# Kernel tuning notes

Hardware: AMD Instinct MI355X
Metric: run time of the kernel (lower is better)

## Reference

```python
import jax, jax.numpy as jnp
import numpy as np

B, L, H = 256, 256, 1024
NUM_HEADS = 16
DIM_PER_HEAD = H // NUM_HEADS  # 64
# faithful to source: scale = (dim_per_head // num_heads) ** -0.5 = (64//16)**-0.5 = 0.5
SCALE = (DIM_PER_HEAD // NUM_HEADS) ** (-0.5)
LN_EPS = 1e-5


def setup_inputs() -> dict:
    key = jax.random.key(0)
    ks = jax.random.split(key, 12)
    s = 1.0 / np.sqrt(H)
    return {
        "key": jax.random.normal(ks[0], (B, L, H), dtype=jnp.float32),
        "value": jax.random.normal(ks[1], (B, L, H), dtype=jnp.float32),
        "query": jax.random.normal(ks[2], (B, 1, H), dtype=jnp.float32),
        "attn_mask": jax.random.randint(ks[3], (B, 1, L), 0, 2).astype(bool),
        "Wq": jax.random.uniform(ks[4], (H, H), jnp.float32, -s, s),
        "bq": jnp.zeros((H,), jnp.float32),
        "Wk": jax.random.uniform(ks[5], (H, H), jnp.float32, -s, s),
        "bk": jnp.zeros((H,), jnp.float32),
        "Wv": jax.random.uniform(ks[6], (H, H), jnp.float32, -s, s),
        "bv": jnp.zeros((H,), jnp.float32),
        "Wf": jax.random.uniform(ks[7], (H, H), jnp.float32, -s, s),
        "bf": jnp.zeros((H,), jnp.float32),
        "gamma": jnp.ones((H,), jnp.float32),
        "beta": jnp.zeros((H,), jnp.float32),
    }


def _split_heads(x):
    # [B, L, H] -> [B, heads, L, d]
    b, l, _ = x.shape
    return x.reshape(b, l, NUM_HEADS, DIM_PER_HEAD).transpose(0, 2, 1, 3)


def reference(key, value, query, attn_mask, Wq, bq, Wk, bk, Wv, bv, Wf, bf, gamma, beta):
    residual = query  # [B, 1, H]
    k = _split_heads(key @ Wk.T + bk)      # [B, h, L, d]
    v = _split_heads(value @ Wv.T + bv)    # [B, h, L, d]
    q = _split_heads(query @ Wq.T + bq)    # [B, h, 1, d]

    scores = jnp.einsum('bhqd,bhkd->bhqk', q, k) * SCALE  # [B, h, 1, L]
    mask = attn_mask[:, None, :, :]                       # [B, 1, 1, L]
    scores = jnp.where(mask, -jnp.inf, scores)
    attention = jax.nn.softmax(scores, axis=-1)           # [B, h, 1, L]

    context = jnp.einsum('bhqk,bhkd->bhqd', attention, v)  # [B, h, 1, d]
    context = context.transpose(0, 2, 1, 3).reshape(query.shape[0], -1, H)  # [B, 1, H]

    out = context @ Wf.T + bf
    x = residual + out
    mu = jnp.mean(x, axis=-1, keepdims=True)
    var = jnp.mean(jnp.square(x - mu), axis=-1, keepdims=True)
    out = (x - mu) * jax.lax.rsqrt(var + LN_EPS) * gamma + beta

    # attention returned as [B*heads, 1, L] like torch bmm layout
    attn_flat = attention.reshape(query.shape[0] * NUM_HEADS, 1, -1)
    return out, attn_flat
```

## Files before the change

kernel.cpp:

```cpp
#include <hip/hip_runtime.h>
#include <math.h>

#define BB 256
#define LL 256
#define HH 1024
#define NH 16
#define DD 64
#define SCALE 0.5f
#define LN_EPS 1e-5f
#define NEG_BIG (-3.402823466e38f)

__global__ __launch_bounds__(256) void t_tr(const float* __restrict__ in,
                                            float* __restrict__ out, int inRS,
                                            int outRS, int inPlane,
                                            int outPlane) {
  __shared__ float lds[64][68];
  const float* ip = in + (size_t)blockIdx.z * inPlane;
  float* op = out + (size_t)blockIdx.z * outPlane;
  const int rt = blockIdx.y, ct = blockIdx.x;
  const int lr = threadIdx.x >> 4;
  const int lc = (threadIdx.x & 15) * 4;
#pragma unroll
  for (int p = 0; p < 4; p++) {
    float4 v = *(const float4*)(ip + (size_t)(rt * 64 + p * 16 + lr) * inRS +
                                ct * 64 + lc);
    *(float4*)(&lds[p * 16 + lr][lc]) = v;
  }
  __syncthreads();
#pragma unroll
  for (int p = 0; p < 4; p++) {
    float4 v = make_float4(lds[lc + 0][p * 16 + lr], lds[lc + 1][p * 16 + lr],
                           lds[lc + 2][p * 16 + lr], lds[lc + 3][p * 16 + lr]);
    *(float4*)(op + (size_t)(ct * 64 + p * 16 + lr) * outRS + rt * 64 + lc) = v;
  }
}

__global__ __launch_bounds__(256) void k1_qproj(const float* __restrict__ Wq,
                                                const float* __restrict__ qTT,
                                                const float* __restrict__ bq,
                                                float* __restrict__ qT) {
  __shared__ float smem[10240];
  const int jt = blockIdx.x;
  const int boff = blockIdx.y * 8;
  const int t = threadIdx.x;
  const int g = __builtin_amdgcn_readfirstlane(t >> 6);
  const int ln = t & 63;
  float* kw = smem + g * 2560;
  const float* Wb = Wq + (size_t)(jt * 64) * HH;
  const int srow = ln >> 2, sc = ln & 3;

  float acc[8];
#pragma unroll
  for (int c = 0; c < 8; c++) acc[c] = 0.f;
  float4 pf[4];
#pragma unroll
  for (int p = 0; p < 4; p++)
    pf[p] = *(const float4*)(Wb + (size_t)(p * 16 + srow) * HH + g * 16 + sc * 4);
  int buf = 0;
  for (int T = 0; T < 16; T++) {
    float* kb = kw + buf * 1280;
#pragma unroll
    for (int p = 0; p < 4; p++)
      *(float4*)(kb + ((p * 16 + srow) * 5 + sc) * 4) = pf[p];
    if (T < 15) {
      const int off = (T + 1) * 64 + g * 16 + sc * 4;
#pragma unroll
      for (int p = 0; p < 4; p++)
        pf[p] = *(const float4*)(Wb + (size_t)(p * 16 + srow) * HH + off);
    }
    const int i0 = T * 64 + g * 16;
#pragma unroll
    for (int u = 0; u < 4; u++) {
      float4 kv = *(const float4*)(kb + (ln * 5 + u) * 4);
      const float* q0 = qTT + (size_t)(i0 + u * 4 + 0) * BB + boff;
      const float* q1 = qTT + (size_t)(i0 + u * 4 + 1) * BB + boff;
      const float* q2 = qTT + (size_t)(i0 + u * 4 + 2) * BB + boff;
      const float* q3 = qTT + (size_t)(i0 + u * 4 + 3) * BB + boff;
#pragma unroll
      for (int c = 0; c < 8; c++) {
        acc[c] = fmaf(kv.x, q0[c], acc[c]);
        acc[c] = fmaf(kv.y, q1[c], acc[c]);
        acc[c] = fmaf(kv.z, q2[c], acc[c]);
        acc[c] = fmaf(kv.w, q3[c], acc[c]);
      }
    }
    buf ^= 1;
  }
  __syncthreads();
  float* part = smem;
  *(float4*)(part + g * 768 + ln * 12 + 0) =
      make_float4(acc[0], acc[1], acc[2], acc[3]);
  *(float4*)(part + g * 768 + ln * 12 + 4) =
      make_float4(acc[4], acc[5], acc[6], acc[7]);
  __syncthreads();
  const int j = t & 63, c0 = (t >> 6) * 2;
  float v0 = 0.f, v1 = 0.f;
#pragma unroll
  for (int g2 = 0; g2 < 4; g2++) {
    v0 += part[g2 * 768 + j * 12 + c0];
    v1 += part[g2 * 768 + j * 12 + c0 + 1];
  }
  const int jg = jt * 64 + j;
  const float bias = bq[jg];
  *(float2*)(qT + (size_t)jg * BB + boff + c0) =
      make_float2(v0 + bias, v1 + bias);
}

__global__ __launch_bounds__(256) void k2_qk(const float* __restrict__ qT,
                                             const float* __restrict__ Wk,
                                             float* __restrict__ qkT) {
  const int h = blockIdx.y;
  const int it = blockIdx.x;
  const int il = threadIdx.x & 63;
  const int bs = __builtin_amdgcn_readfirstlane(threadIdx.x >> 6);
  const int i = it * 64 + il;
  const int boff = blockIdx.z * 64 + bs * 16;
  float acc[16];
#pragma unroll
  for (int k = 0; k < 16; k++) acc[k] = 0.f;
#pragma unroll 2
  for (int d = 0; d < DD; d++) {
    float wv = Wk[(size_t)(h * DD + d) * HH + i];
    const float* qrow = qT + (h * DD + d) * BB + boff;
#pragma unroll
    for (int k = 0; k < 16; k++) acc[k] = fmaf(qrow[k], wv, acc[k]);
  }
#pragma unroll
  for (int k = 0; k < 16; k++)
    qkT[(size_t)((boff + k) * NH + h) * HH + i] = SCALE * acc[k];
}

__global__ __launch_bounds__(256) void k2b_relayout(
    const float* __restrict__ qkT, float* __restrict__ qkR) {
  __shared__ float lds[16][268];
  const int b = blockIdx.y, seg = blockIdx.x;
  const int t = threadIdx.x;
  const int row = t >> 4, l16 = t & 15;
  const float* src = qkT + (size_t)b * 16384 + row * HH + seg * 256 + l16 * 16;
#pragma unroll
  for (int p = 0; p < 4; p++)
    *(float4*)(&lds[row][l16 * 16 + p * 4]) = *(const float4*)(src + p * 4);
  __syncthreads();
  const int c = t & 63;
  const int i4g = t >> 6;
  const int h = c >> 2, i3 = c & 3;
  float* dst = qkR + (size_t)b * 16384 + seg * 4096;
#pragma unroll
  for (int jj = 0; jj < 16; jj++) {
    const int i4l = i4g * 16 + jj;
    dst[i4l * 64 + c] = lds[h][i4l * 4 + i3];
  }
}

__global__ __launch_bounds__(256, 4) void k3a_scores(
    const float* __restrict__ key, const int* __restrict__ mask,
    const float* __restrict__ qkR, float* __restrict__ scoresT) {
  __shared__ float part[5120];
  const int b = blockIdx.y;
  const int lt = blockIdx.x;
  const int t = threadIdx.x;
  const int g = __builtin_amdgcn_readfirstlane(t >> 6);
  const int ln = t & 63;
  const float* keyrow = key + ((size_t)(b * LL + lt * 64 + ln)) * HH + g * 256;
  const float* qkb = qkR + (size_t)b * 16384 + g * 4096;

  float acc[16];
#pragma unroll
  for (int h = 0; h < NH; h++) acc[h] = 0.f;

  float4 p0 = *(const float4*)(keyrow + 0);
  float4 p1 = *(const float4*)(keyrow + 4);
  float4 p2 = *(const float4*)(keyrow + 8);
  float4 p3 = *(const float4*)(keyrow + 12);

  for (int c = 0; c < 16; c++) {
    float4 k0 = p0, k1 = p1, k2 = p2, k3 = p3;
    if (c < 15) {
      const float* nx = keyrow + (c + 1) * 16;
      p0 = *(const float4*)(nx + 0);
      p1 = *(const float4*)(nx + 4);
      p2 = *(const float4*)(nx + 8);
      p3 = *(const float4*)(nx + 12);
    }
    const float* q = qkb + c * 256;
#pragma unroll
    for (int h = 0; h < NH; h++) {
      const float* qh = q + h * 4;
      acc[h] = fmaf(k0.x, qh[0], acc[h]);
      acc[h] = fmaf(k0.y, qh[1], acc[h]);
      acc[h] = fmaf(k0.z, qh[2], acc[h]);
      acc[h] = fmaf(k0.w, qh[3], acc[h]);
      acc[h] = fmaf(k1.x, qh[64], acc[h]);
      acc[h] = fmaf(k1.y, qh[65], acc[h]);
      acc[h] = fmaf(k1.z, qh[66], acc[h]);
      acc[h] = fmaf(k1.w, qh[67], acc[h]);
      acc[h] = fmaf(k2.x, qh[128], acc[h]);
      acc[h] = fmaf(k2.y, qh[129], acc[h]);
      acc[h] = fmaf(k2.z, qh[130], acc[h]);
      acc[h] = fmaf(k2.w, qh[131], acc[h]);
      acc[h] = fmaf(k3.x, qh[192], acc[h]);
      acc[h] = fmaf(k3.y, qh[193], acc[h]);
      acc[h] = fmaf(k3.z, qh[194], acc[h]);
      acc[h] = fmaf(k3.w, qh[195], acc[h]);
    }
  }

#pragma unroll
  for (int u = 0; u < 4; u++)
    *(float4*)(part + (g * 64 + ln) * 20 + u * 4) =
        make_float4(acc[u * 4], acc[u * 4 + 1], acc[u * 4 + 2], acc[u * 4 + 3]);
  __syncthreads();
  const int row = t & 63, hq = t >> 6;
  float4 s0 = *(const float4*)(part + (0 * 64 + row) * 20 + hq * 4);
  float4 s1 = *(const float4*)(part + (1 * 64 + row) * 20 + hq * 4);
  float4 s2 = *(const float4*)(part + (2 * 64 + row) * 20 + hq * 4);
  float4 s3 = *(const float4*)(part + (3 * 64 + row) * 20 + hq * 4);
  const int l = lt * 64 + row;
  const int mk = mask[b * LL + l];
  float o0 = mk ? NEG_BIG : (s0.x + s1.x + s2.x + s3.x);
  float o1 = mk ? NEG_BIG : (s0.y + s1.y + s2.y + s3.y);
  float o2 = mk ? NEG_BIG : (s0.z + s1.z + s2.z + s3.z);
  float o3 = mk ? NEG_BIG : (s0.w + s1.w + s2.w + s3.w);
  scoresT[(size_t)(b * NH + hq * 4 + 0) * LL + l] = o0;
  scoresT[(size_t)(b * NH + hq * 4 + 1) * LL + l] = o1;
  scoresT[(size_t)(b * NH + hq * 4 + 2) * LL + l] = o2;
  scoresT[(size_t)(b * NH + hq * 4 + 3) * LL + l] = o3;
}

__global__ __launch_bounds__(256) void k3b_softmax(float* __restrict__ attn) {
  const int r = blockIdx.x * 4 + (threadIdx.x >> 6);
  const int lane = threadIdx.x & 63;
  float* rowp = attn + (size_t)r * LL;
  float4 s = *(const float4*)(rowp + lane * 4);
  float m = fmaxf(fmaxf(s.x, s.y), fmaxf(s.z, s.w));
#pragma unroll
  for (int off = 32; off >= 1; off >>= 1) m = fmaxf(m, __shfl_xor(m, off));
  float ex = __expf(s.x - m), ey = __expf(s.y - m), ez = __expf(s.z - m),
        ew = __expf(s.w - m);
  float e = ex + ey + ez + ew;
#pragma unroll
  for (int off = 32; off >= 1; off >>= 1) e += __shfl_xor(e, off);
  float inv = 1.0f / e;
  *(float4*)(rowp + lane * 4) = make_float4(ex * inv, ey * inv, ez * inv, ew * inv);
}

__global__ __launch_bounds__(256, 4) void k3c_vbar(
    const float* __restrict__ value, const float* __restrict__ attn,
    float* __restrict__ vbar) {
  const int b = blockIdx.y;
  const int d = blockIdx.x * 256 + threadIdx.x;
  const float* ab = attn + (size_t)b * NH * LL;
  const float* valb = value + (size_t)b * LL * HH + d;
  float acc[16];
#pragma unroll
  for (int h = 0; h < NH; h++) acc[h] = 0.f;
  for (int l0 = 0; l0 < LL; l0 += 16) {
    float vv[16];
#pragma unroll
    for (int k = 0; k < 16; k++) vv[k] = valb[(size_t)(l0 + k) * HH];
#pragma unroll
    for (int h = 0; h < NH; h++) {
      const float4* ar = (const float4*)(ab + h * LL + l0);
      float4 a0 = ar[0], a1 = ar[1], a2 = ar[2], a3 = ar[3];
      acc[h] = fmaf(a0.x, vv[0], acc[h]);
      acc[h] = fmaf(a0.y, vv[1], acc[h]);
      acc[h] = fmaf(a0.z, vv[2], acc[h]);
      acc[h] = fmaf(a0.w, vv[3], acc[h]);
      acc[h] = fmaf(a1.x, vv[4], acc[h]);
      acc[h] = fmaf(a1.y, vv[5], acc[h]);
      acc[h] = fmaf(a1.z, vv[6], acc[h]);
      acc[h] = fmaf(a1.w, vv[7], acc[h]);
      acc[h] = fmaf(a2.x, vv[8], acc[h]);
      acc[h] = fmaf(a2.y, vv[9], acc[h]);
      acc[h] = fmaf(a2.z, vv[10], acc[h]);
      acc[h] = fmaf(a2.w, vv[11], acc[h]);
      acc[h] = fmaf(a3.x, vv[12], acc[h]);
      acc[h] = fmaf(a3.y, vv[13], acc[h]);
      acc[h] = fmaf(a3.z, vv[14], acc[h]);
      acc[h] = fmaf(a3.w, vv[15], acc[h]);
    }
  }
#pragma unroll
  for (int h = 0; h < NH; h++)
    vbar[((size_t)b * NH + h) * HH + d] = acc[h];
}

__global__ __launch_bounds__(256) void k4_ctx(const float* __restrict__ Wv,
                                              const float* __restrict__ vbarT,
                                              const float* __restrict__ bv,
                                              float* __restrict__ ctxT) {
  __shared__ float smem[10240];
  const int jt = blockIdx.x;
  const int boff = blockIdx.y * 8;
  const int t = threadIdx.x;
  const int g = __builtin_amdgcn_readfirstlane(t >> 6);
  const int ln = t & 63;
  float* kw = smem + g * 2560;
  const float* Wb = Wv + (size_t)(jt * 64) * HH;
  const float* vt = vbarT + (size_t)jt * HH * BB;
  const int srow = ln >> 2, sc = ln & 3;

  float acc[8];
#pragma unroll
  for (int c = 0; c < 8; c++) acc[c] = 0.f;
  float4 pf[4];
#pragma unroll
  for (int p = 0; p < 4; p++)
    pf[p] = *(const float4*)(Wb + (size_t)(p * 16 + srow) * HH + g * 16 + sc * 4);
  int buf = 0;
  for (int T = 0; T < 16; T++) {
    float* kb = kw + buf * 1280;
#pragma unroll
    for (int p = 0; p < 4; p++)
      *(float4*)(kb + ((p * 16 + srow) * 5 + sc) * 4) = pf[p];
    if (T < 15) {
      const int off = (T + 1) * 64 + g * 16 + sc * 4;
#pragma unroll
      for (int p = 0; p < 4; p++)
        pf[p] = *(const float4*)(Wb + (size_t)(p * 16 + srow) * HH + off);
    }
    const int i0 = T * 64 + g * 16;
#pragma unroll
    for (int u = 0; u < 4; u++) {
      float4 kv = *(const float4*)(kb + (ln * 5 + u) * 4);
      const float* q0 = vt + (size_t)(i0 + u * 4 + 0) * BB + boff;
      const float* q1 = vt + (size_t)(i0 + u * 4 + 1) * BB + boff;
      const float* q2 = vt + (size_t)(i0 + u * 4 + 2) * BB + boff;
      const float* q3 = vt + (size_t)(i0 + u * 4 + 3) * BB + boff;
#pragma unroll
      for (int c = 0; c < 8; c++) {
        acc[c] = fmaf(kv.x, q0[c], acc[c]);
        acc[c] = fmaf(kv.y, q1[c], acc[c]);
        acc[c] = fmaf(kv.z, q2[c], acc[c]);
        acc[c] = fmaf(kv.w, q3[c], acc[c]);
      }
    }
    buf ^= 1;
  }
  __syncthreads();
  float* part = smem;
  *(float4*)(part + g * 768 + ln * 12 + 0) =
      make_float4(acc[0], acc[1], acc[2], acc[3]);
  *(float4*)(part + g * 768 + ln * 12 + 4) =
      make_float4(acc[4], acc[5], acc[6], acc[7]);
  __syncthreads();
  const int j = t & 63, c0 = (t >> 6) * 2;
  float v0 = 0.f, v1 = 0.f;
#pragma unroll
  for (int g2 = 0; g2 < 4; g2++) {
    v0 += part[g2 * 768 + j * 12 + c0];
    v1 += part[g2 * 768 + j * 12 + c0 + 1];
  }
  const int jg = jt * 64 + j;
  const float bias = bv[jg];
  *(float2*)(ctxT + (size_t)jg * BB + boff + c0) =
      make_float2(v0 + bias, v1 + bias);
}

__global__ __launch_bounds__(256) void k5_outproj(
    const float* __restrict__ Wf, const float* __restrict__ ctxT,
    const float* __restrict__ bf, const float* __restrict__ query,
    float* __restrict__ xws) {
  __shared__ float smem[10240];
  const int jt = blockIdx.x;
  const int boff = blockIdx.y * 8;
  const int t = threadIdx.x;
  const int g = __builtin_amdgcn_readfirstlane(t >> 6);
  const int ln = t & 63;
  float* kw = smem + g * 2560;
  const float* Wb = Wf + (size_t)(jt * 64) * HH;
  const int srow = ln >> 2, sc = ln & 3;

  float acc[8];
#pragma unroll
  for (int c = 0; c < 8; c++) acc[c] = 0.f;
  float4 pf[4];
#pragma unroll
  for (int p = 0; p < 4; p++)
    pf[p] = *(const float4*)(Wb + (size_t)(p * 16 + srow) * HH + g * 16 + sc * 4);
  int buf = 0;
  for (int T = 0; T < 16; T++) {
    float* kb = kw + buf * 1280;
#pragma unroll
    for (int p = 0; p < 4; p++)
      *(float4*)(kb + ((p * 16 + srow) * 5 + sc) * 4) = pf[p];
    if (T < 15) {
      const int off = (T + 1) * 64 + g * 16 + sc * 4;
#pragma unroll
      for (int p = 0; p < 4; p++)
        pf[p] = *(const float4*)(Wb + (size_t)(p * 16 + srow) * HH + off);
    }
    const int i0 = T * 64 + g * 16;
#pragma unroll
    for (int u = 0; u < 4; u++) {
      float4 kv = *(const float4*)(kb + (ln * 5 + u) * 4);
      const float* q0 = ctxT + (size_t)(i0 + u * 4 + 0) * BB + boff;
      const float* q1 = ctxT + (size_t)(i0 + u * 4 + 1) * BB + boff;
      const float* q2 = ctxT + (size_t)(i0 + u * 4 + 2) * BB + boff;
      const float* q3 = ctxT + (size_t)(i0 + u * 4 + 3) * BB + boff;
#pragma unroll
      for (int c = 0; c < 8; c++) {
        acc[c] = fmaf(kv.x, q0[c], acc[c]);
        acc[c] = fmaf(kv.y, q1[c], acc[c]);
        acc[c] = fmaf(kv.z, q2[c], acc[c]);
        acc[c] = fmaf(kv.w, q3[c], acc[c]);
      }
    }
    buf ^= 1;
  }
  __syncthreads();
  float* part = smem;
  *(float4*)(part + g * 768 + ln * 12 + 0) =
      make_float4(acc[0], acc[1], acc[2], acc[3]);
  *(float4*)(part + g * 768 + ln * 12 + 4) =
      make_float4(acc[4], acc[5], acc[6], acc[7]);
  __syncthreads();
  const int j = t & 63, c0 = (t >> 6) * 2;
  float v0 = 0.f, v1 = 0.f;
#pragma unroll
  for (int g2 = 0; g2 < 4; g2++) {
    v0 += part[g2 * 768 + j * 12 + c0];
    v1 += part[g2 * 768 + j * 12 + c0 + 1];
  }
  const int jg = jt * 64 + j;
  const float bias = bf[jg];
  const int b0 = boff + c0;
  xws[(size_t)b0 * HH + jg] = v0 + bias + query[(size_t)b0 * HH + jg];
  xws[(size_t)(b0 + 1) * HH + jg] = v1 + bias + query[(size_t)(b0 + 1) * HH + jg];
}

__global__ __launch_bounds__(256) void k6_ln(const float* __restrict__ xws,
                                             const float* __restrict__ gamma,
                                             const float* __restrict__ beta,
                                             float* __restrict__ out0) {
  __shared__ float rb[8];
  const int b = blockIdx.x, t = threadIdx.x;
  float4 v = *(const float4*)(xws + (size_t)b * HH + 4 * t);
  float s = v.x + v.y + v.z + v.w;
#pragma unroll
  for (int off = 32; off >= 1; off >>= 1) s += __shfl_xor(s, off);
  if ((t & 63) == 0) rb[t >> 6] = s;
  __syncthreads();
  float mu = (rb[0] + rb[1] + rb[2] + rb[3]) * (1.0f / HH);
  float dx = v.x - mu, dy = v.y - mu, dz = v.z - mu, dw = v.w - mu;
  float q = dx * dx + dy * dy + dz * dz + dw * dw;
#pragma unroll
  for (int off = 32; off >= 1; off >>= 1) q += __shfl_xor(q, off);
  if ((t & 63) == 0) rb[4 + (t >> 6)] = q;
  __syncthreads();
  float var = (rb[4] + rb[5] + rb[6] + rb[7]) * (1.0f / HH);
  float rs = rsqrtf(var + LN_EPS);
  float4 gm = *(const float4*)(gamma + 4 * t);
  float4 bt = *(const float4*)(beta + 4 * t);
  float4 o;
  o.x = dx * rs * gm.x + bt.x;
  o.y = dy * rs * gm.y + bt.y;
  o.z = dz * rs * gm.z + bt.z;
  o.w = dw * rs * gm.w + bt.w;
  *(float4*)(out0 + (size_t)b * HH + 4 * t) = o;
}

extern "C" void kernel_launch(void* const* d_in, const int* in_sizes, int n_in,
                              void* d_out, int out_size, void* d_ws,
                              size_t ws_size, hipStream_t stream) {
  (void)in_sizes; (void)n_in; (void)out_size; (void)ws_size;
  const float* key = (const float*)d_in[0];
  const float* value = (const float*)d_in[1];
  const float* query = (const float*)d_in[2];
  const int* mask = (const int*)d_in[3];
  const float* Wq = (const float*)d_in[4];
  const float* bq = (const float*)d_in[5];
  const float* Wk = (const float*)d_in[6];
  const float* Wv = (const float*)d_in[8];
  const float* bv = (const float*)d_in[9];
  const float* Wf = (const float*)d_in[10];
  const float* bf = (const float*)d_in[11];
  const float* gamma = (const float*)d_in[12];
  const float* beta = (const float*)d_in[13];

  float* out0 = (float*)d_out;
  float* attnOut = out0 + BB * HH;

  char* ws = (char*)d_ws;
  float* qT = (float*)(ws);
  float* qTT = (float*)(ws + (1 << 20));
  float* qkT = (float*)(ws + (2 << 20));
  float* qkR = (float*)(ws + (18 << 20));
  float* vbar = (float*)(ws + (2 << 20));
  float* vbarT = (float*)(ws + (34 << 20));
  float* ctxT = (float*)(ws);
  float* xws = (float*)(ws + (1 << 20));

  t_tr<<<dim3(16, 4, 1), 256, 0, stream>>>(query, qTT, HH, BB, 0, 0);
  k1_qproj<<<dim3(16, 32), 256, 0, stream>>>(Wq, qTT, bq, qT);
  k2_qk<<<dim3(16, 16, 4), 256, 0, stream>>>(qT, Wk, qkT);
  k2b_relayout<<<dim3(4, 256), 256, 0, stream>>>(qkT, qkR);
  k3a_scores<<<dim3(4, 256), 256, 0, stream>>>(key, mask, qkR, attnOut);
  k3b_softmax<<<dim3(1024), 256, 0, stream>>>(attnOut);
  k3c_vbar<<<dim3(4, 256), 256, 0, stream>>>(value, attnOut, vbar);
  t_tr<<<dim3(16, 4, 16), 256, 0, stream>>>(vbar, vbarT, NH * HH, BB, HH,
                                            HH * BB);
  k4_ctx<<<dim3(16, 32), 256, 0, stream>>>(Wv, vbarT, bv, ctxT);
  k5_outproj<<<dim3(16, 32), 256, 0, stream>>>(Wf, ctxT, bf, query, xws);
  k6_ln<<<dim3(256), 256, 0, stream>>>(xws, gamma, beta, out0);
}
```

Baseline: 358.8 us.

## Drop qk relayout kernel and regroup scores and vbar work by head group

Removes the separate relayout pass over the q·Wk product. The scores kernel now reads the product directly, staging it through double-buffered LDS per wave, and each wave owns 4 heads across the full hidden dimension, so the cross-wave LDS reduction and block barrier go away. The vbar kernel stages attention weights in LDS and splits heads across waves with a finer grid over d. This saves a kernel launch and an extra pass over global memory, but the 4 waves in a block now read the same key and value rows, so these large streamed inputs are fetched redundantly and rely on cache hits.

```diff
diff --git a/kernel.cpp b/kernel.cpp
--- a/kernel.cpp
+++ b/kernel.cpp
@@ -130,101 +130,88 @@
     qkT[(size_t)((boff + k) * NH + h) * HH + i] = SCALE * acc[k];
 }
 
-__global__ __launch_bounds__(256) void k2b_relayout(
-    const float* __restrict__ qkT, float* __restrict__ qkR) {
-  __shared__ float lds[16][268];
-  const int b = blockIdx.y, seg = blockIdx.x;
-  const int t = threadIdx.x;
-  const int row = t >> 4, l16 = t & 15;
-  const float* src = qkT + (size_t)b * 16384 + row * HH + seg * 256 + l16 * 16;
-#pragma unroll
-  for (int p = 0; p < 4; p++)
-    *(float4*)(&lds[row][l16 * 16 + p * 4]) = *(const float4*)(src + p * 4);
-  __syncthreads();
-  const int c = t & 63;
-  const int i4g = t >> 6;
-  const int h = c >> 2, i3 = c & 3;
-  float* dst = qkR + (size_t)b * 16384 + seg * 4096;
-#pragma unroll
-  for (int jj = 0; jj < 16; jj++) {
-    const int i4l = i4g * 16 + jj;
-    dst[i4l * 64 + c] = lds[h][i4l * 4 + i3];
-  }
-}
-
 __global__ __launch_bounds__(256, 4) void k3a_scores(
     const float* __restrict__ key, const int* __restrict__ mask,
-    const float* __restrict__ qkR, float* __restrict__ scoresT) {
-  __shared__ float part[5120];
+    const float* __restrict__ qkT, float* __restrict__ scoresT) {
+  __shared__ float qlds[2][4096];
   const int b = blockIdx.y;
   const int lt = blockIdx.x;
   const int t = threadIdx.x;
   const int g = __builtin_amdgcn_readfirstlane(t >> 6);
   const int ln = t & 63;
-  const float* keyrow = key + ((size_t)(b * LL + lt * 64 + ln)) * HH + g * 256;
-  const float* qkb = qkR + (size_t)b * 16384 + g * 4096;
-
-  float acc[16];
-#pragma unroll
-  for (int h = 0; h < NH; h++) acc[h] = 0.f;
+  const float* qksrc = qkT + (size_t)b * 16384 +
+                       (size_t)(g * 4 + (ln >> 4)) * HH + (ln & 15) * 16;
+
+  const int l = lt * 64 + ln;
+  const float* keyrow = key + ((size_t)b * LL + l) * HH;
+
+  float acc[4] = {0.f, 0.f, 0.f, 0.f};
+
+  float4 qf[4];
+#pragma unroll
+  for (int p = 0; p < 4; p++) qf[p] = *(const float4*)(qksrc + p * 4);
 
   float4 p0 = *(const float4*)(keyrow + 0);
   float4 p1 = *(const float4*)(keyrow + 4);
   float4 p2 = *(const float4*)(keyrow + 8);
   float4 p3 = *(const float4*)(keyrow + 12);
 
-  for (int c = 0; c < 16; c++) {
-    float4 k0 = p0, k1 = p1, k2 = p2, k3 = p3;
-    if (c < 15) {
-      const float* nx = keyrow + (c + 1) * 16;
-      p0 = *(const float4*)(nx + 0);
-      p1 = *(const float4*)(nx + 4);
-      p2 = *(const float4*)(nx + 8);
-      p3 = *(const float4*)(nx + 12);
-    }
-    const float* q = qkb + c * 256;
-#pragma unroll
-    for (int h = 0; h < NH; h++) {
-      const float* qh = q + h * 4;
-      acc[h] = fmaf(k0.x, qh[0], acc[h]);
-      acc[h] = fmaf(k0.y, qh[1], acc[h]);
-      acc[h] = fmaf(k0.z, qh[2], acc[h]);
-      acc[h] = fmaf(k0.w, qh[3], acc[h]);
-      acc[h] = fmaf(k1.x, qh[64], acc[h]);
-      acc[h] = fmaf(k1.y, qh[65], acc[h]);
-      acc[h] = fmaf(k1.z, qh[66], acc[h]);
-      acc[h] = fmaf(k1.w, qh[67], acc[h]);
-      acc[h] = fmaf(k2.x, qh[128], acc[h]);
-      acc[h] = fmaf(k2.y, qh[129], acc[h]);
-      acc[h] = fmaf(k2.z, qh[130], acc[h]);
-      acc[h] = fmaf(k2.w, qh[131], acc[h]);
-      acc[h] = fmaf(k3.x, qh[192], acc[h]);
-      acc[h] = fmaf(k3.y, qh[193], acc[h]);
-      acc[h] = fmaf(k3.z, qh[194], acc[h]);
-      acc[h] = fmaf(k3.w, qh[195], acc[h]);
-    }
-  }
-
-#pragma unroll
-  for (int u = 0; u < 4; u++)
-    *(float4*)(part + (g * 64 + ln) * 20 + u * 4) =
-        make_float4(acc[u * 4], acc[u * 4 + 1], acc[u * 4 + 2], acc[u * 4 + 3]);
-  __syncthreads();
-  const int row = t & 63, hq = t >> 6;
-  float4 s0 = *(const float4*)(part + (0 * 64 + row) * 20 + hq * 4);
-  float4 s1 = *(const float4*)(part + (1 * 64 + row) * 20 + hq * 4);
-  float4 s2 = *(const float4*)(part + (2 * 64 + row) * 20 + hq * 4);
-  float4 s3 = *(const float4*)(part + (3 * 64 + row) * 20 + hq * 4);
-  const int l = lt * 64 + row;
+  for (int s = 0; s < 4; s++) {
+    float* base = qlds[s & 1] + g * 1024;
+#pragma unroll
+    for (int p = 0; p < 4; p++)
+      *(float4*)(base + ln * 16 + p * 4) = qf[p];
+    if (s < 3) {
+#pragma unroll
+      for (int p = 0; p < 4; p++)
+        qf[p] = *(const float4*)(qksrc + (s + 1) * 256 + p * 4);
+    }
+#pragma unroll 2
+    for (int c = 0; c < 16; c++) {
+      const int cc = s * 16 + c;
+      float4 k0 = p0, k1 = p1, k2 = p2, k3 = p3;
+      if (cc < 63) {
+        const float* nx = keyrow + (cc + 1) * 16;
+        p0 = *(const float4*)(nx + 0);
+        p1 = *(const float4*)(nx + 4);
+        p2 = *(const float4*)(nx + 8);
+        p3 = *(const float4*)(nx + 12);
+      }
+#pragma unroll
+      for (int hh = 0; hh < 4; hh++) {
+        const float* qr = base + hh * 256 + c * 16;
+        float4 a0 = *(const float4*)(qr + 0);
+        float4 a1 = *(const float4*)(qr + 4);
+        float4 a2 = *(const float4*)(qr + 8);
+        float4 a3 = *(const float4*)(qr + 12);
+        float s2 = acc[hh];
+        s2 = fmaf(k0.x, a0.x, s2);
+        s2 = fmaf(k0.y, a0.y, s2);
+        s2 = fmaf(k0.z, a0.z, s2);
+        s2 = fmaf(k0.w, a0.w, s2);
+        s2 = fmaf(k1.x, a1.x, s2);
+        s2 = fmaf(k1.y, a1.y, s2);
+        s2 = fmaf(k1.z, a1.z, s2);
+        s2 = fmaf(k1.w, a1.w, s2);
+        s2 = fmaf(k2.x, a2.x, s2);
+        s2 = fmaf(k2.y, a2.y, s2);
+        s2 = fmaf(k2.z, a2.z, s2);
+        s2 = fmaf(k2.w, a2.w, s2);
+        s2 = fmaf(k3.x, a3.x, s2);
+        s2 = fmaf(k3.y, a3.y, s2);
+        s2 = fmaf(k3.z, a3.z, s2);
+        s2 = fmaf(k3.w, a3.w, s2);
+        acc[hh] = s2;
+      }
+    }
+  }
+
   const int mk = mask[b * LL + l];
-  float o0 = mk ? NEG_BIG : (s0.x + s1.x + s2.x + s3.x);
-  float o1 = mk ? NEG_BIG : (s0.y + s1.y + s2.y + s3.y);
-  float o2 = mk ? NEG_BIG : (s0.z + s1.z + s2.z + s3.z);
-  float o3 = mk ? NEG_BIG : (s0.w + s1.w + s2.w + s3.w);
-  scoresT[(size_t)(b * NH + hq * 4 + 0) * LL + l] = o0;
-  scoresT[(size_t)(b * NH + hq * 4 + 1) * LL + l] = o1;
-  scoresT[(size_t)(b * NH + hq * 4 + 2) * LL + l] = o2;
-  scoresT[(size_t)(b * NH + hq * 4 + 3) * LL + l] = o3;
+#pragma unroll
+  for (int hh = 0; hh < 4; hh++) {
+    float v = mk ? NEG_BIG : acc[hh];
+    scoresT[((size_t)b * NH + g * 4 + hh) * LL + l] = v;
+  }
 }
 
 __global__ __launch_bounds__(256) void k3b_softmax(float* __restrict__ attn) {
@@ -247,42 +234,59 @@
 __global__ __launch_bounds__(256, 4) void k3c_vbar(
     const float* __restrict__ value, const float* __restrict__ attn,
     float* __restrict__ vbar) {
+  __shared__ float alds[4096];
   const int b = blockIdx.y;
-  const int d = blockIdx.x * 256 + threadIdx.x;
-  const float* ab = attn + (size_t)b * NH * LL;
+  const int dt = blockIdx.x;
+  const int t = threadIdx.x;
+  const int g = __builtin_amdgcn_readfirstlane(t >> 6);
+  const int ln = t & 63;
+  const float* ab = attn + (size_t)b * 4096;
+#pragma unroll
+  for (int j = 0; j < 4; j++)
+    *(float4*)(alds + j * 1024 + t * 4) =
+        *(const float4*)(ab + j * 1024 + t * 4);
+  __syncthreads();
+
+  const int d = dt * 64 + ln;
   const float* valb = value + (size_t)b * LL * HH + d;
-  float acc[16];
-#pragma unroll
-  for (int h = 0; h < NH; h++) acc[h] = 0.f;
+  const float* aw = alds + (g * 4) * 256;
+
+  float acc[4] = {0.f, 0.f, 0.f, 0.f};
+
   for (int l0 = 0; l0 < LL; l0 += 16) {
     float vv[16];
 #pragma unroll
     for (int k = 0; k < 16; k++) vv[k] = valb[(size_t)(l0 + k) * HH];
 #pragma unroll
-    for (int h = 0; h < NH; h++) {
-      const float4* ar = (const float4*)(ab + h * LL + l0);
-      float4 a0 = ar[0], a1 = ar[1], a2 = ar[2], a3 = ar[3];
-      acc[h] = fmaf(a0.x, vv[0], acc[h]);
-      acc[h] = fmaf(a0.y, vv[1], acc[h]);
-      acc[h] = fmaf(a0.z, vv[2], acc[h]);
-      acc[h] = fmaf(a0.w, vv[3], acc[h]);
-      acc[h] = fmaf(a1.x, vv[4], acc[h]);
-      acc[h] = fmaf(a1.y, vv[5], acc[h]);
-      acc[h] = fmaf(a1.z, vv[6], acc[h]);
-      acc[h] = fmaf(a1.w, vv[7], acc[h]);
-      acc[h] = fmaf(a2.x, vv[8], acc[h]);
-      acc[h] = fmaf(a2.y, vv[9], acc[h]);
-      acc[h] = fmaf(a2.z, vv[10], acc[h]);
-      acc[h] = fmaf(a2.w, vv[11], acc[h]);
-      acc[h] = fmaf(a3.x, vv[12], acc[h]);
-      acc[h] = fmaf(a3.y, vv[13], acc[h]);
-      acc[h] = fmaf(a3.z, vv[14], acc[h]);
-      acc[h] = fmaf(a3.w, vv[15], acc[h]);
-    }
-  }
-#pragma unroll
-  for (int h = 0; h < NH; h++)
-    vbar[((size_t)b * NH + h) * HH + d] = acc[h];
+    for (int hh = 0; hh < 4; hh++) {
+      const float* ar = aw + hh * 256 + l0;
+      float4 a0 = *(const float4*)(ar + 0);
+      float4 a1 = *(const float4*)(ar + 4);
+      float4 a2 = *(const float4*)(ar + 8);
+      float4 a3 = *(const float4*)(ar + 12);
+      float s = acc[hh];
+      s = fmaf(a0.x, vv[0], s);
+      s = fmaf(a0.y, vv[1], s);
+      s = fmaf(a0.z, vv[2], s);
+      s = fmaf(a0.w, vv[3], s);
+      s = fmaf(a1.x, vv[4], s);
+      s = fmaf(a1.y, vv[5], s);
+      s = fmaf(a1.z, vv[6], s);
+      s = fmaf(a1.w, vv[7], s);
+      s = fmaf(a2.x, vv[8], s);
+      s = fmaf(a2.y, vv[9], s);
+      s = fmaf(a2.z, vv[10], s);
+      s = fmaf(a2.w, vv[11], s);
+      s = fmaf(a3.x, vv[12], s);
+      s = fmaf(a3.y, vv[13], s);
+      s = fmaf(a3.z, vv[14], s);
+      s = fmaf(a3.w, vv[15], s);
+      acc[hh] = s;
+    }
+  }
+#pragma unroll
+  for (int hh = 0; hh < 4; hh++)
+    vbar[((size_t)b * NH + g * 4 + hh) * HH + d] = acc[hh];
 }
 
 __global__ __launch_bounds__(256) void k4_ctx(const float* __restrict__ Wv,
@@ -485,8 +489,7 @@
   float* qT = (float*)(ws);
   float* qTT = (float*)(ws + (1 << 20));
   float* qkT = (float*)(ws + (2 << 20));
-  float* qkR = (float*)(ws + (18 << 20));
-  float* vbar = (float*)(ws + (2 << 20));
+  float* vbar = (float*)(ws + (18 << 20));
   float* vbarT = (float*)(ws + (34 << 20));
   float* ctxT = (float*)(ws);
   float* xws = (float*)(ws + (1 << 20));
@@ -494,10 +497,9 @@
   t_tr<<<dim3(16, 4, 1), 256, 0, stream>>>(query, qTT, HH, BB, 0, 0);
   k1_qproj<<<dim3(16, 32), 256, 0, stream>>>(Wq, qTT, bq, qT);
   k2_qk<<<dim3(16, 16, 4), 256, 0, stream>>>(qT, Wk, qkT);
-  k2b_relayout<<<dim3(4, 256), 256, 0, stream>>>(qkT, qkR);
-  k3a_scores<<<dim3(4, 256), 256, 0, stream>>>(key, mask, qkR, attnOut);
+  k3a_scores<<<dim3(4, 256), 256, 0, stream>>>(key, mask, qkT, attnOut);
   k3b_softmax<<<dim3(1024), 256, 0, stream>>>(attnOut);
-  k3c_vbar<<<dim3(4, 256), 256, 0, stream>>>(value, attnOut, vbar);
+  k3c_vbar<<<dim3(16, 256), 256, 0, stream>>>(value, attnOut, vbar);
   t_tr<<<dim3(16, 4, 16), 256, 0, stream>>>(vbar, vbarT, NH * HH, BB, HH,
                                             HH * BB);
   k4_ctx<<<dim3(16, 32), 256, 0, stream>>>(Wv, vbarT, bv, ctxT);
```

New measurement: 413.1 us. +15.1%, slower.

## Restage scores and attention-value kernels through LDS with register tiling

Applied to the files above, without the earlier changes.

The scores kernel now loads key and query-projection tiles with coalesced float4 reads into double-buffered LDS, computes a 4x4 register tile per thread, and reduces partial sums with cross-lane shuffles in place of an LDS partial-sum buffer. The attention-times-value kernel caches the batch's attention rows in LDS and has each thread compute 4 columns by 4 heads with float4 value loads and software prefetch. Both changes aim to cut redundant global loads of broadcast operands and to make the key/value streams coalesced. In exchange they add LDS traffic and barriers, and the dropped occupancy hint may change register allocation.

```diff
diff --git a/kernel.cpp b/kernel.cpp
--- a/kernel.cpp
+++ b/kernel.cpp
@@ -9,6 +9,12 @@
 #define SCALE 0.5f
 #define LN_EPS 1e-5f
 #define NEG_BIG (-3.402823466e38f)
+
+#define FMA4(accv, vq, s)                \
+  accv.x = fmaf(vq.x, s, accv.x);       \
+  accv.y = fmaf(vq.y, s, accv.y);       \
+  accv.z = fmaf(vq.z, s, accv.z);       \
+  accv.w = fmaf(vq.w, s, accv.w);
 
 __global__ __launch_bounds__(256) void t_tr(const float* __restrict__ in,
                                             float* __restrict__ out, int inRS,
@@ -152,79 +158,101 @@
   }
 }
 
-__global__ __launch_bounds__(256, 4) void k3a_scores(
+__global__ __launch_bounds__(256) void k3a_scores(
     const float* __restrict__ key, const int* __restrict__ mask,
     const float* __restrict__ qkR, float* __restrict__ scoresT) {
-  __shared__ float part[5120];
+  __shared__ float klds[2][64 * 68];
+  __shared__ float qlds[2][1024];
   const int b = blockIdx.y;
   const int lt = blockIdx.x;
   const int t = threadIdx.x;
   const int g = __builtin_amdgcn_readfirstlane(t >> 6);
   const int ln = t & 63;
-  const float* keyrow = key + ((size_t)(b * LL + lt * 64 + ln)) * HH + g * 256;
-  const float* qkb = qkR + (size_t)b * 16384 + g * 4096;
-
-  float acc[16];
-#pragma unroll
-  for (int h = 0; h < NH; h++) acc[h] = 0.f;
-
-  float4 p0 = *(const float4*)(keyrow + 0);
-  float4 p1 = *(const float4*)(keyrow + 4);
-  float4 p2 = *(const float4*)(keyrow + 8);
-  float4 p3 = *(const float4*)(keyrow + 12);
+  const int m15 = ln & 15;
+  const int g4 = ln >> 4;
+  const int srow = t >> 4;
+  const int sc4 = (t & 15) * 4;
+
+  const float* keyb = key + ((size_t)(b * LL + lt * 64)) * HH;
+  const float* qkb = qkR + (size_t)b * 16384;
+
+  float acc[4][4];
+#pragma unroll
+  for (int r = 0; r < 4; r++)
+#pragma unroll
+    for (int h = 0; h < 4; h++) acc[r][h] = 0.f;
+
+  float4 kf[4];
+#pragma unroll
+  for (int p = 0; p < 4; p++)
+    kf[p] = *(const float4*)(keyb + (size_t)(srow + 16 * p) * HH + sc4);
+  float4 qf = *(const float4*)(qkb + t * 4);
 
   for (int c = 0; c < 16; c++) {
-    float4 k0 = p0, k1 = p1, k2 = p2, k3 = p3;
+    float* kb = klds[c & 1];
+    float* qb = qlds[c & 1];
+#pragma unroll
+    for (int p = 0; p < 4; p++)
+      *(float4*)(kb + (srow + 16 * p) * 68 + sc4) = kf[p];
+    *(float4*)(qb + t * 4) = qf;
     if (c < 15) {
-      const float* nx = keyrow + (c + 1) * 16;
-      p0 = *(const float4*)(nx + 0);
-      p1 = *(const float4*)(nx + 4);
-      p2 = *(const float4*)(nx + 8);
-      p3 = *(const float4*)(nx + 12);
-    }
-    const float* q = qkb + c * 256;
-#pragma unroll
-    for (int h = 0; h < NH; h++) {
-      const float* qh = q + h * 4;
-      acc[h] = fmaf(k0.x, qh[0], acc[h]);
-      acc[h] = fmaf(k0.y, qh[1], acc[h]);
-      acc[h] = fmaf(k0.z, qh[2], acc[h]);
-      acc[h] = fmaf(k0.w, qh[3], acc[h]);
-      acc[h] = fmaf(k1.x, qh[64], acc[h]);
-      acc[h] = fmaf(k1.y, qh[65], acc[h]);
-      acc[h] = fmaf(k1.z, qh[66], acc[h]);
-      acc[h] = fmaf(k1.w, qh[67], acc[h]);
-      acc[h] = fmaf(k2.x, qh[128], acc[h]);
-      acc[h] = fmaf(k2.y, qh[129], acc[h]);
-      acc[h] = fmaf(k2.z, qh[130], acc[h]);
-      acc[h] = fmaf(k2.w, qh[131], acc[h]);
-      acc[h] = fmaf(k3.x, qh[192], acc[h]);
-      acc[h] = fmaf(k3.y, qh[193], acc[h]);
-      acc[h] = fmaf(k3.z, qh[194], acc[h]);
-      acc[h] = fmaf(k3.w, qh[195], acc[h]);
-    }
-  }
-
-#pragma unroll
-  for (int u = 0; u < 4; u++)
-    *(float4*)(part + (g * 64 + ln) * 20 + u * 4) =
-        make_float4(acc[u * 4], acc[u * 4 + 1], acc[u * 4 + 2], acc[u * 4 + 3]);
-  __syncthreads();
-  const int row = t & 63, hq = t >> 6;
-  float4 s0 = *(const float4*)(part + (0 * 64 + row) * 20 + hq * 4);
-  float4 s1 = *(const float4*)(part + (1 * 64 + row) * 20 + hq * 4);
-  float4 s2 = *(const float4*)(part + (2 * 64 + row) * 20 + hq * 4);
-  float4 s3 = *(const float4*)(part + (3 * 64 + row) * 20 + hq * 4);
-  const int l = lt * 64 + row;
+      const int ioff = 64 * (c + 1);
+#pragma unroll
+      for (int p = 0; p < 4; p++)
+        kf[p] = *(const float4*)(keyb + (size_t)(srow + 16 * p) * HH + ioff + sc4);
+      qf = *(const float4*)(qkb + 1024 * (c + 1) + t * 4);
+    }
+    __syncthreads();
+#pragma unroll
+    for (int iq = 0; iq < 4; iq++) {
+      const int iqf = g4 * 4 + iq;
+      const float* qu = qb + iqf * 64 + g * 16;
+      float4 q0 = *(const float4*)(qu + 0);
+      float4 q1 = *(const float4*)(qu + 4);
+      float4 q2 = *(const float4*)(qu + 8);
+      float4 q3 = *(const float4*)(qu + 12);
+      const int il = g4 * 16 + iq * 4;
+#pragma unroll
+      for (int r = 0; r < 4; r++) {
+        float4 kv = *(const float4*)(kb + (m15 + 16 * r) * 68 + il);
+        acc[r][0] = fmaf(kv.x, q0.x, acc[r][0]);
+        acc[r][0] = fmaf(kv.y, q0.y, acc[r][0]);
+        acc[r][0] = fmaf(kv.z, q0.z, acc[r][0]);
+        acc[r][0] = fmaf(kv.w, q0.w, acc[r][0]);
+        acc[r][1] = fmaf(kv.x, q1.x, acc[r][1]);
+        acc[r][1] = fmaf(kv.y, q1.y, acc[r][1]);
+        acc[r][1] = fmaf(kv.z, q1.z, acc[r][1]);
+        acc[r][1] = fmaf(kv.w, q1.w, acc[r][1]);
+        acc[r][2] = fmaf(kv.x, q2.x, acc[r][2]);
+        acc[r][2] = fmaf(kv.y, q2.y, acc[r][2]);
+        acc[r][2] = fmaf(kv.z, q2.z, acc[r][2]);
+        acc[r][2] = fmaf(kv.w, q2.w, acc[r][2]);
+        acc[r][3] = fmaf(kv.x, q3.x, acc[r][3]);
+        acc[r][3] = fmaf(kv.y, q3.y, acc[r][3]);
+        acc[r][3] = fmaf(kv.z, q3.z, acc[r][3]);
+        acc[r][3] = fmaf(kv.w, q3.w, acc[r][3]);
+      }
+    }
+  }
+
+#pragma unroll
+  for (int r = 0; r < 4; r++)
+#pragma unroll
+    for (int h = 0; h < 4; h++) {
+      acc[r][h] += __shfl_xor(acc[r][h], 16);
+      acc[r][h] += __shfl_xor(acc[r][h], 32);
+    }
+
+  const int l = lt * 64 + 16 * g4 + m15;
   const int mk = mask[b * LL + l];
-  float o0 = mk ? NEG_BIG : (s0.x + s1.x + s2.x + s3.x);
-  float o1 = mk ? NEG_BIG : (s0.y + s1.y + s2.y + s3.y);
-  float o2 = mk ? NEG_BIG : (s0.z + s1.z + s2.z + s3.z);
-  float o3 = mk ? NEG_BIG : (s0.w + s1.w + s2.w + s3.w);
-  scoresT[(size_t)(b * NH + hq * 4 + 0) * LL + l] = o0;
-  scoresT[(size_t)(b * NH + hq * 4 + 1) * LL + l] = o1;
-  scoresT[(size_t)(b * NH + hq * 4 + 2) * LL + l] = o2;
-  scoresT[(size_t)(b * NH + hq * 4 + 3) * LL + l] = o3;
+  float o0 = mk ? NEG_BIG : acc[g4][0];
+  float o1 = mk ? NEG_BIG : acc[g4][1];
+  float o2 = mk ? NEG_BIG : acc[g4][2];
+  float o3 = mk ? NEG_BIG : acc[g4][3];
+  scoresT[((size_t)(b * NH + g * 4 + 0)) * LL + l] = o0;
+  scoresT[((size_t)(b * NH + g * 4 + 1)) * LL + l] = o1;
+  scoresT[((size_t)(b * NH + g * 4 + 2)) * LL + l] = o2;
+  scoresT[((size_t)(b * NH + g * 4 + 3)) * LL + l] = o3;
 }
 
 __global__ __launch_bounds__(256) void k3b_softmax(float* __restrict__ attn) {
@@ -244,45 +272,54 @@
   *(float4*)(rowp + lane * 4) = make_float4(ex * inv, ey * inv, ez * inv, ew * inv);
 }
 
-__global__ __launch_bounds__(256, 4) void k3c_vbar(
+__global__ __launch_bounds__(256) void k3c_vbar(
     const float* __restrict__ value, const float* __restrict__ attn,
     float* __restrict__ vbar) {
+  __shared__ float alds[4096];
   const int b = blockIdx.y;
-  const int d = blockIdx.x * 256 + threadIdx.x;
-  const float* ab = attn + (size_t)b * NH * LL;
-  const float* valb = value + (size_t)b * LL * HH + d;
-  float acc[16];
-#pragma unroll
-  for (int h = 0; h < NH; h++) acc[h] = 0.f;
-  for (int l0 = 0; l0 < LL; l0 += 16) {
-    float vv[16];
-#pragma unroll
-    for (int k = 0; k < 16; k++) vv[k] = valb[(size_t)(l0 + k) * HH];
-#pragma unroll
-    for (int h = 0; h < NH; h++) {
-      const float4* ar = (const float4*)(ab + h * LL + l0);
-      float4 a0 = ar[0], a1 = ar[1], a2 = ar[2], a3 = ar[3];
-      acc[h] = fmaf(a0.x, vv[0], acc[h]);
-      acc[h] = fmaf(a0.y, vv[1], acc[h]);
-      acc[h] = fmaf(a0.z, vv[2], acc[h]);
-      acc[h] = fmaf(a0.w, vv[3], acc[h]);
-      acc[h] = fmaf(a1.x, vv[4], acc[h]);
-      acc[h] = fmaf(a1.y, vv[5], acc[h]);
-      acc[h] = fmaf(a1.z, vv[6], acc[h]);
-      acc[h] = fmaf(a1.w, vv[7], acc[h]);
-      acc[h] = fmaf(a2.x, vv[8], acc[h]);
-      acc[h] = fmaf(a2.y, vv[9], acc[h]);
-      acc[h] = fmaf(a2.z, vv[10], acc[h]);
-      acc[h] = fmaf(a2.w, vv[11], acc[h]);
-      acc[h] = fmaf(a3.x, vv[12], acc[h]);
-      acc[h] = fmaf(a3.y, vv[13], acc[h]);
-      acc[h] = fmaf(a3.z, vv[14], acc[h]);
-      acc[h] = fmaf(a3.w, vv[15], acc[h]);
-    }
-  }
-#pragma unroll
-  for (int h = 0; h < NH; h++)
-    vbar[((size_t)b * NH + h) * HH + d] = acc[h];
+  const int dt = blockIdx.x;
+  const int t = threadIdx.x;
+  const int g = __builtin_amdgcn_readfirstlane(t >> 6);
+  const int ln = t & 63;
+  const float* ab = attn + (size_t)b * 4096;
+#pragma unroll
+  for (int j = 0; j < 4; j++)
+    *(float4*)(alds + j * 1024 + t * 4) = *(const float4*)(ab + j * 1024 + t * 4);
+  __syncthreads();
+
+  const int d0 = dt * 256 + ln * 4;
+  const float* valb = value + (size_t)b * LL * HH + d0;
+  const float* aw = alds + g * 4 * 256;
+
+  float4 ac0 = make_float4(0.f, 0.f, 0.f, 0.f);
+  float4 ac1 = ac0, ac2 = ac0, ac3 = ac0;
+
+  float4 vf[4];
+#pragma unroll
+  for (int q = 0; q < 4; q++) vf[q] = *(const float4*)(valb + (size_t)q * HH);
+
+#pragma unroll 4
+  for (int lq = 0; lq < 64; lq++) {
+    float4 v0 = vf[0], v1 = vf[1], v2 = vf[2], v3 = vf[3];
+    if (lq < 63) {
+#pragma unroll
+      for (int q = 0; q < 4; q++)
+        vf[q] = *(const float4*)(valb + (size_t)((lq + 1) * 4 + q) * HH);
+    }
+    float4 a0 = *(const float4*)(aw + 0 * 256 + lq * 4);
+    float4 a1 = *(const float4*)(aw + 1 * 256 + lq * 4);
+    float4 a2 = *(const float4*)(aw + 2 * 256 + lq * 4);
+    float4 a3 = *(const float4*)(aw + 3 * 256 + lq * 4);
+    FMA4(ac0, v0, a0.x); FMA4(ac0, v1, a0.y); FMA4(ac0, v2, a0.z); FMA4(ac0, v3, a0.w);
+    FMA4(ac1, v0, a1.x); FMA4(ac1, v1, a1.y); FMA4(ac1, v2, a1.z); FMA4(ac1, v3, a1.w);
+    FMA4(ac2, v0, a2.x); FMA4(ac2, v1, a2.y); FMA4(ac2, v2, a2.z); FMA4(ac2, v3, a2.w);
+    FMA4(ac3, v0, a3.x); FMA4(ac3, v1, a3.y); FMA4(ac3, v2, a3.z); FMA4(ac3, v3, a3.w);
+  }
+  float* vb = vbar + ((size_t)(b * NH + g * 4)) * HH + d0;
+  *(float4*)(vb + 0 * HH) = ac0;
+  *(float4*)(vb + 1 * HH) = ac1;
+  *(float4*)(vb + 2 * HH) = ac2;
+  *(float4*)(vb + 3 * HH) = ac3;
 }
 
 __global__ __launch_bounds__(256) void k4_ctx(const float* __restrict__ Wv,
```

New measurement: 430.9 us. 1.2x slower.
